# Kernel tuning notes

Hardware: AMD Instinct MI355X
Metric: run time of the kernel (lower is better)

## Reference

```python
import jax, jax.numpy as jnp
import numpy as np
import math

H = 16          # num heads
D = 64          # size_per_head
HID = H * D     # 1024
ROT = 32        # rotary_hsize <= D//2


def setup_inputs() -> dict:
    key = jax.random.key(0)
    ks = jax.random.split(key, 10)
    B, S = 2, 2048
    x = jax.random.normal(ks[0], (B, S, HID), dtype=jnp.float32)
    sinusoids = jax.random.normal(ks[1], (B, 2, S, ROT), dtype=jnp.float32)
    attention_bias = jnp.zeros((B, 1, S, S), dtype=jnp.float32)
    scale = 1.0 / math.sqrt(HID)
    Wq = jax.random.normal(ks[2], (HID, HID), dtype=jnp.float32) * scale
    bq = jnp.zeros((HID,), dtype=jnp.float32)
    Wk = jax.random.normal(ks[3], (HID, HID), dtype=jnp.float32) * scale
    bk = jnp.zeros((HID,), dtype=jnp.float32)
    Wv = jax.random.normal(ks[4], (HID, HID), dtype=jnp.float32) * scale
    bv = jnp.zeros((HID,), dtype=jnp.float32)
    Wo = jax.random.normal(ks[5], (HID, HID), dtype=jnp.float32) * scale
    return {"x": x, "sinusoids": sinusoids, "attention_bias": attention_bias,
            "Wq": Wq, "bq": bq, "Wk": Wk, "bk": bk, "Wv": Wv, "bv": bv, "Wo": Wo}


def _apply_rotary(qk, sin, cos):
    # qk: [B,S,H,D]; sin/cos: [B,S,1,ROT]
    r = qk[..., :ROT]
    # stack([-even, odd], -1).reshape -> interleaved (-x0, x1, -x2, x3, ...)
    rt = jnp.stack([-r[..., ::2], r[..., 1::2]], axis=-1).reshape(r.shape)
    return jnp.concatenate([r * cos + rt * sin, qk[..., ROT:]], axis=-1)


def reference(x, sinusoids, attention_bias, Wq, bq, Wk, bk, Wv, bv, Wo):
    B, S, _ = x.shape
    q = (x @ Wq + bq).reshape(B, S, H, D)
    k = (x @ Wk + bk).reshape(B, S, H, D)
    v = (x @ Wv + bv).reshape(B, S, H, D)
    sin = sinusoids[..., 0, :, None, :]  # [B,S,1,ROT]
    cos = sinusoids[..., 1, :, None, :]
    q = _apply_rotary(q, sin, cos)
    k = _apply_rotary(k, sin, cos)
    q = q / math.sqrt(D)
    scores = jnp.einsum('bqhd,bkhd->bhqk', q, k) + attention_bias
    probs = jax.nn.softmax(scores, axis=-1)
    out = jnp.einsum('bhqk,bkhd->bqhd', probs, v).reshape(B, S, HID)
    return out @ Wo
```

## Files before the change

### kernel.cpp

```cpp
#include <hip/hip_runtime.h>
#include <hip/hip_bf16.h>

#define H_   16
#define D_   64
#define HID  1024
#define S_   2048
#define B_   2
#define M_   (B_*S_)
#define ROT  32
#define LOG2E 1.44269504088896341f
#define QSCALE (0.125f * LOG2E)

typedef __bf16 bf16x8 __attribute__((ext_vector_type(8)));
typedef float  f32x4  __attribute__((ext_vector_type(4)));

#define XB_OFF   0u
#define WQT_OFF  (8u<<20)
#define WKT_OFF  (10u<<20)
#define WVT_OFF  (12u<<20)
#define WOT_OFF  (14u<<20)
#define F_OFF    (16u<<20)
#define QH_OFF   ((16u<<20) + (1u<<19))
#define KH_OFF   (QH_OFF + (8u<<20))
#define VT_OFF   (KH_OFF + (8u<<20))
#define AB_OFF   (VT_OFF + (8u<<20))

__device__ __forceinline__ float fexp2(float x) {
#if __has_builtin(__builtin_amdgcn_exp2f)
  return __builtin_amdgcn_exp2f(x);
#else
  return __expf(x * 0.69314718055994531f);
#endif
}

__device__ __forceinline__ unsigned pk2(float a, float b) {
  union { unsigned u; __bf16 h[2]; } w;
  w.h[0] = (__bf16)a; w.h[1] = (__bf16)b;
  return w.u;
}

__global__ __launch_bounds__(256) void prep_kernel(const float* __restrict__ x,
                                                   const float* __restrict__ sinu,
                                                   const float* __restrict__ abias,
                                                   const float* __restrict__ W0, const float* __restrict__ W1,
                                                   const float* __restrict__ W2, const float* __restrict__ W3,
                                                   __hip_bfloat16* __restrict__ xb,
                                                   float* __restrict__ F,
                                                   __hip_bfloat16* __restrict__ T0, __hip_bfloat16* __restrict__ T1,
                                                   __hip_bfloat16* __restrict__ T2, __hip_bfloat16* __restrict__ T3,
                                                   int* __restrict__ flag) {
  __shared__ float tile[32][33];
  int idx = blockIdx.x;
  int tid = threadIdx.x;
  if (idx < 4096) {
    int i = (idx * 256 + tid) * 4;
    float4 v = *(const float4*)(x + i);
    union { __hip_bfloat16 h[4]; uint2 u; } o;
    o.h[0] = __float2bfloat16(v.x);
    o.h[1] = __float2bfloat16(v.y);
    o.h[2] = __float2bfloat16(v.z);
    o.h[3] = __float2bfloat16(v.w);
    *(uint2*)(xb + i) = o.u;
  } else if (idx < 4608) {
    int i = (idx - 4096) * 256 + tid;
    int d  = i & (ROT-1);
    int bs = i >> 5;
    int s  = bs & (S_-1);
    int b  = bs >> 11;
    float sn = sinu[(((size_t)b*2 + 0)*S_ + s)*ROT + d];
    float cs = sinu[(((size_t)b*2 + 1)*S_ + s)*ROT + d];
    F[i] = cs + ((d & 1) ? sn : -sn);
  } else if (idx < 8704) {
    int widx = idx - 4608;
    int z    = widx >> 10;
    int rem  = widx & 1023;
    const float* W = (z==0) ? W0 : (z==1) ? W1 : (z==2) ? W2 : W3;
    __hip_bfloat16* T = (z==0) ? T0 : (z==1) ? T1 : (z==2) ? T2 : T3;
    int bx = (rem & 31) * 32;
    int by = (rem >> 5) * 32;
    int tx = tid & 31, ty = tid >> 5;
    #pragma unroll
    for (int i = 0; i < 4; i++)
      tile[ty + i*8][tx] = W[(size_t)(by + ty + i*8)*HID + bx + tx];
    __syncthreads();
    #pragma unroll
    for (int i = 0; i < 4; i++)
      T[(size_t)(bx + ty + i*8)*HID + by + tx] = __float2bfloat16(tile[tx][ty + i*8]);
  } else {
    size_t i = ((size_t)(idx - 8704) * 256 + tid) * 16;
    const uint4* p = (const uint4*)(abias + i);
    unsigned acc = 0;
    #pragma unroll
    for (int j = 0; j < 4; j++) {
      uint4 u = p[j];
      acc |= u.x | u.y | u.z | u.w;
    }
    if (acc) *flag = 1;
  }
}

template<int MODE>
__global__ __launch_bounds__(256) void gemm128(const __hip_bfloat16* __restrict__ A,
                                               const __hip_bfloat16* __restrict__ Bt,
                                               const float* __restrict__ bq,
                                               const float* __restrict__ bk,
                                               const float* __restrict__ bv,
                                               const float* __restrict__ F,
                                               __hip_bfloat16* __restrict__ Qh,
                                               __hip_bfloat16* __restrict__ Kh,
                                               __hip_bfloat16* __restrict__ Vt,
                                               float* __restrict__ outf) {
  __shared__ __align__(16) __bf16 Asm[2][128*32];
  __shared__ __align__(16) __bf16 Bsm[2][128*32];
  int tid  = threadIdx.x;
  int lane = tid & 63;
  int wv   = tid >> 6;
  int lr   = lane & 15;
  int qd   = lane >> 4;
  int row0 = blockIdx.y * 128;
  int col0 = blockIdx.x * 128;
  int wrow = (wv >> 1) * 64;
  int wcol = (wv & 1) * 64;

  int cg = ((tid & 3) ^ ((tid >> 2) & 3)) * 8;
  const __bf16* Ag = (const __bf16*)A  + (size_t)(row0 + (tid >> 2)) * HID + cg;
  const __bf16* Bg = (const __bf16*)Bt + (size_t)(col0 + (tid >> 2)) * HID + cg;

  f32x4 acc[4][4] = {};

  auto stage = [&](int buf, int k0) {
    __builtin_amdgcn_global_load_lds(Ag + k0,                  &Asm[buf][wv*512],        16, 0, 0);
    __builtin_amdgcn_global_load_lds(Ag + (size_t)64*HID + k0, &Asm[buf][2048 + wv*512], 16, 0, 0);
    __builtin_amdgcn_global_load_lds(Bg + k0,                  &Bsm[buf][wv*512],        16, 0, 0);
    __builtin_amdgcn_global_load_lds(Bg + (size_t)64*HID + k0, &Bsm[buf][2048 + wv*512], 16, 0, 0);
  };

  stage(0, 0);
  int buf = 0;
  for (int k0 = 0; k0 < HID; k0 += 32, buf ^= 1) {
    __syncthreads();
    if (k0 + 32 < HID) stage(buf ^ 1, k0 + 32);
    const __bf16* As = &Asm[buf][0];
    const __bf16* Bs = &Bsm[buf][0];
    bf16x8 a[4], b[4];
    #pragma unroll
    for (int i = 0; i < 4; i++) {
      int row = wrow + i*16 + lr;
      a[i] = *(const bf16x8*)(As + row*32 + ((qd ^ (row & 3)) * 8));
    }
    #pragma unroll
    for (int t = 0; t < 4; t++) {
      int row = wcol + t*16 + lr;
      b[t] = *(const bf16x8*)(Bs + row*32 + ((qd ^ (row & 3)) * 8));
    }
    #pragma unroll
    for (int i = 0; i < 4; i++)
      #pragma unroll
      for (int t = 0; t < 4; t++)
        acc[i][t] = __builtin_amdgcn_mfma_f32_16x16x32_bf16(a[i], b[t], acc[i][t], 0, 0, 0);
  }

  if (MODE == 1) {
    #pragma unroll
    for (int i = 0; i < 4; i++)
      #pragma unroll
      for (int t = 0; t < 4; t++)
        #pragma unroll
        for (int r = 0; r < 4; r++) {
          int m = row0 + wrow + i*16 + qd*4 + r;
          int n = col0 + wcol + t*16 + lr;
          outf[(size_t)m*HID + n] = acc[i][t][r];
        }
    return;
  }

  int proj = col0 >> 10;
  int nb   = (col0 & 1023) + wcol;
  const float* bias = (proj == 0) ? bq : ((proj == 1) ? bk : bv);
  #pragma unroll
  for (int i = 0; i < 4; i++) {
    #pragma unroll
    for (int t = 0; t < 4; t++) {
      int nl = nb + t*16 + lr;
      int h  = nl >> 6, d = nl & 63;
      if (proj == 2) {
        int m0 = row0 + wrow + i*16 + qd*4;
        int b2 = m0 >> 11, s0 = m0 & (S_-1);
        union { uint2 u; __bf16 hh[4]; } w;
        #pragma unroll
        for (int r = 0; r < 4; r++)
          w.hh[r] = (__bf16)(acc[i][t][r] + bias[nl]);
        *(uint2*)((__bf16*)Vt + ((size_t)(b2*H_ + h)*D_ + d)*S_ + s0) = w.u;
      } else {
        __hip_bfloat16* dst = (proj == 0) ? Qh : Kh;
        #pragma unroll
        for (int r = 0; r < 4; r++) {
          int m = row0 + wrow + i*16 + qd*4 + r;
          int b2 = m >> 11, s = m & (S_-1);
          float v = acc[i][t][r] + bias[nl];
          if (d < ROT) v *= F[(size_t)(b2*S_ + s)*ROT + d];
          if (proj == 0) v *= QSCALE;
          dst[((size_t)(b2*H_ + h)*S_ + s)*D_ + d] = __float2bfloat16(v);
        }
      }
    }
  }
}

#define PSTRIDE 72
__global__ __launch_bounds__(256) void flash_kernel(const __hip_bfloat16* __restrict__ Qh,
                                                    const __hip_bfloat16* __restrict__ Kh,
                                                    const __hip_bfloat16* __restrict__ Vt,
                                                    const float* __restrict__ abias,
                                                    const int* __restrict__ flag,
                                                    __hip_bfloat16* __restrict__ Ab) {
  __shared__ __align__(16) __bf16 Ksm[2][64*64];
  __shared__ __align__(16) __bf16 Vsm[2][64*64];
  __shared__ __align__(16) __bf16 Pb[4][32*PSTRIDE];
  int tid  = threadIdx.x;
  int lane = tid & 63;
  int wv   = tid >> 6;
  int lr   = lane & 15;
  int qd   = lane >> 4;
  int idx  = blockIdx.x;
  int xcd  = idx & 7;
  int slot = idx >> 3;
  int bh   = xcd * 4 + (slot >> 4);
  int qblk = slot & 15;
  int b  = bh >> 4;
  int h  = bh & 15;
  int q0 = qblk * 128 + wv * 32;

  const __bf16* Kbase = (const __bf16*)Kh + (size_t)bh*S_*D_;
  const __bf16* Vbase = (const __bf16*)Vt + (size_t)bh*D_*S_;

  const __bf16* Qp = (const __bf16*)Qh + ((size_t)bh*S_ + q0 + lr)*D_ + qd*8;
  bf16x8 qa00 = *(const bf16x8*)(Qp);
  bf16x8 qa01 = *(const bf16x8*)(Qp + 32);
  bf16x8 qa10 = *(const bf16x8*)(Qp + 16*D_);
  bf16x8 qa11 = *(const bf16x8*)(Qp + 16*D_ + 32);

  int hasbias = *flag;
  const float* bp0 = abias + (size_t)b*S_*S_ + (size_t)(q0 + lr)*S_;
  const float* bp1 = bp0 + (size_t)16*S_;

  int rowb = tid >> 3;
  int cg8  = ((tid & 7) ^ (rowb & 7)) * 8;

  auto stageKV = [&](int bf, int kt2) {
    __builtin_amdgcn_global_load_lds(Kbase + (size_t)(kt2 + rowb)*D_ + cg8,      &Ksm[bf][wv*512],        16, 0, 0);
    __builtin_amdgcn_global_load_lds(Kbase + (size_t)(kt2 + 32 + rowb)*D_ + cg8, &Ksm[bf][2048 + wv*512], 16, 0, 0);
    __builtin_amdgcn_global_load_lds(Vbase + (size_t)rowb*S_ + kt2 + cg8,        &Vsm[bf][wv*512],        16, 0, 0);
    __builtin_amdgcn_global_load_lds(Vbase + (size_t)(32 + rowb)*S_ + kt2 + cg8, &Vsm[bf][2048 + wv*512], 16, 0, 0);
  };

  f32x4 oacc0[4] = {}, oacc1[4] = {};
  float lsum0 = 0.f, lsum1 = 0.f;
  __bf16* P = &Pb[wv][0];
  int sw = lr & 7;

  stageKV(0, 0);
  int buf = 0;
  for (int kt = 0; kt < S_; kt += 64, buf ^= 1) {
    __syncthreads();
    if (kt + 64 < S_) stageKV(buf ^ 1, kt + 64);

    bf16x8 kf0[4], kf1[4];
    #pragma unroll
    for (int c = 0; c < 4; c++) {
      const __bf16* Kr = &Ksm[buf][(c*16 + lr)*64];
      kf0[c] = *(const bf16x8*)(Kr + ((qd       ^ sw) * 8));
      kf1[c] = *(const bf16x8*)(Kr + (((4 + qd) ^ sw) * 8));
    }
    f32x4 s0[4], s1[4];
    #pragma unroll
    for (int c = 0; c < 4; c++) {
      f32x4 z = {};
      z     = __builtin_amdgcn_mfma_f32_16x16x32_bf16(kf0[c], qa00, z, 0, 0, 0);
      s0[c] = __builtin_amdgcn_mfma_f32_16x16x32_bf16(kf1[c], qa01, z, 0, 0, 0);
      f32x4 z2 = {};
      z2    = __builtin_amdgcn_mfma_f32_16x16x32_bf16(kf0[c], qa10, z2, 0, 0, 0);
      s1[c] = __builtin_amdgcn_mfma_f32_16x16x32_bf16(kf1[c], qa11, z2, 0, 0, 0);
    }
    bf16x8 vf0[4], vf1[4];
    #pragma unroll
    for (int t = 0; t < 4; t++) {
      const __bf16* Vr = &Vsm[buf][(t*16 + lr)*64];
      vf0[t] = *(const bf16x8*)(Vr + ((qd       ^ sw) * 8));
      vf1[t] = *(const bf16x8*)(Vr + (((4 + qd) ^ sw) * 8));
    }
    if (hasbias) {
      #pragma unroll
      for (int c = 0; c < 4; c++) {
        float4 b0 = *(const float4*)(bp0 + kt + c*16 + qd*4);
        float4 b1 = *(const float4*)(bp1 + kt + c*16 + qd*4);
        s0[c][0] += b0.x*LOG2E; s0[c][1] += b0.y*LOG2E; s0[c][2] += b0.z*LOG2E; s0[c][3] += b0.w*LOG2E;
        s1[c][0] += b1.x*LOG2E; s1[c][1] += b1.y*LOG2E; s1[c][2] += b1.z*LOG2E; s1[c][3] += b1.w*LOG2E;
      }
    }
    #pragma unroll
    for (int c = 0; c < 4; c++) {
      float p0 = fexp2(s0[c][0]), p1 = fexp2(s0[c][1]), p2 = fexp2(s0[c][2]), p3 = fexp2(s0[c][3]);
      lsum0 += (p0 + p1) + (p2 + p3);
      *(unsigned*)(P + lr*PSTRIDE + c*16 + qd*4)     = pk2(p0, p1);
      *(unsigned*)(P + lr*PSTRIDE + c*16 + qd*4 + 2) = pk2(p2, p3);
      float r0 = fexp2(s1[c][0]), r1 = fexp2(s1[c][1]), r2 = fexp2(s1[c][2]), r3 = fexp2(s1[c][3]);
      lsum1 += (r0 + r1) + (r2 + r3);
      *(unsigned*)(P + (16+lr)*PSTRIDE + c*16 + qd*4)     = pk2(r0, r1);
      *(unsigned*)(P + (16+lr)*PSTRIDE + c*16 + qd*4 + 2) = pk2(r2, r3);
    }
    asm volatile("s_waitcnt lgkmcnt(0)" ::: "memory");
    bf16x8 pb00 = *(const bf16x8*)(P + lr*PSTRIDE + qd*8);
    bf16x8 pb01 = *(const bf16x8*)(P + lr*PSTRIDE + 32 + qd*8);
    bf16x8 pb10 = *(const bf16x8*)(P + (16+lr)*PSTRIDE + qd*8);
    bf16x8 pb11 = *(const bf16x8*)(P + (16+lr)*PSTRIDE + 32 + qd*8);
    #pragma unroll
    for (int t = 0; t < 4; t++) {
      oacc0[t] = __builtin_amdgcn_mfma_f32_16x16x32_bf16(vf0[t], pb00, oacc0[t], 0, 0, 0);
      oacc0[t] = __builtin_amdgcn_mfma_f32_16x16x32_bf16(vf1[t], pb01, oacc0[t], 0, 0, 0);
      oacc1[t] = __builtin_amdgcn_mfma_f32_16x16x32_bf16(vf0[t], pb10, oacc1[t], 0, 0, 0);
      oacc1[t] = __builtin_amdgcn_mfma_f32_16x16x32_bf16(vf1[t], pb11, oacc1[t], 0, 0, 0);
    }
  }

  lsum0 += __shfl_xor(lsum0, 16); lsum0 += __shfl_xor(lsum0, 32);
  lsum1 += __shfl_xor(lsum1, 16); lsum1 += __shfl_xor(lsum1, 32);
  float inv0 = 1.0f / lsum0;
  float inv1 = 1.0f / lsum1;
  size_t ro0 = ((size_t)(b*S_ + q0 + lr))*HID + h*D_;
  size_t ro1 = ((size_t)(b*S_ + q0 + 16 + lr))*HID + h*D_;
  #pragma unroll
  for (int t = 0; t < 4; t++) {
    union { uint2 u; __bf16 hh[4]; } w0, w1;
    #pragma unroll
    for (int r = 0; r < 4; r++) {
      w0.hh[r] = (__bf16)(oacc0[t][r]*inv0);
      w1.hh[r] = (__bf16)(oacc1[t][r]*inv1);
    }
    *(uint2*)((__bf16*)Ab + ro0 + t*16 + qd*4) = w0.u;
    *(uint2*)((__bf16*)Ab + ro1 + t*16 + qd*4) = w1.u;
  }
}

extern "C" void kernel_launch(void* const* d_in, const int* in_sizes, int n_in,
                              void* d_out, int out_size, void* d_ws, size_t ws_size,
                              hipStream_t stream) {
  (void)in_sizes; (void)n_in; (void)out_size; (void)ws_size;
  const float* x     = (const float*)d_in[0];
  const float* sinu  = (const float*)d_in[1];
  const float* abias = (const float*)d_in[2];
  const float* Wq    = (const float*)d_in[3];
  const float* bq    = (const float*)d_in[4];
  const float* Wk    = (const float*)d_in[5];
  const float* bk    = (const float*)d_in[6];
  const float* Wv    = (const float*)d_in[7];
  const float* bv    = (const float*)d_in[8];
  const float* Wo    = (const float*)d_in[9];

  char* ws = (char*)d_ws;
  __hip_bfloat16* Xb  = (__hip_bfloat16*)(ws + XB_OFF);
  __hip_bfloat16* Wqt = (__hip_bfloat16*)(ws + WQT_OFF);
  __hip_bfloat16* Wkt = (__hip_bfloat16*)(ws + WKT_OFF);
  __hip_bfloat16* Wvt = (__hip_bfloat16*)(ws + WVT_OFF);
  __hip_bfloat16* Wot = (__hip_bfloat16*)(ws + WOT_OFF);
  float*          F   = (float*)(ws + F_OFF);
  __hip_bfloat16* Qh  = (__hip_bfloat16*)(ws + QH_OFF);
  __hip_bfloat16* Kh  = (__hip_bfloat16*)(ws + KH_OFF);
  __hip_bfloat16* Vt  = (__hip_bfloat16*)(ws + VT_OFF);
  __hip_bfloat16* Ab  = (__hip_bfloat16*)(ws + AB_OFF);
  int* flag = (int*)d_out;

  hipMemsetAsync(flag, 0, 4, stream);
  prep_kernel<<<10752, 256, 0, stream>>>(x, sinu, abias, Wq, Wk, Wv, Wo,
                                         Xb, F, Wqt, Wkt, Wvt, Wot, flag);

  gemm128<0><<<dim3(3*HID/128, M_/128), 256, 0, stream>>>(
      Xb, Wqt, bq, bk, bv, F, Qh, Kh, Vt, nullptr);

  flash_kernel<<<dim3(512), 256, 0, stream>>>(Qh, Kh, Vt, abias, flag, Ab);

  gemm128<1><<<dim3(HID/128, M_/128), 256, 0, stream>>>(
      Ab, Wot, nullptr, nullptr, nullptr, nullptr, nullptr, nullptr, nullptr, (float*)d_out);
}
```

Before: 229.7 us.

## Software-pipeline PV matmul in flash kernel and use 128x64 tiles for output GEMM

The flash kernel now double-buffers the P tile in LDS and defers each block's P·V MFMAs to the next iteration. They run after the next QK^T scores are computed, so exp/pack work can overlap with matrix ops and the lgkmcnt wait inside the loop goes away. The output projection is split into its own kernel with 128x64 tiles, doubling the block count for better CU occupancy on the 8x32 grid. This costs more LDS for the P buffers and extra V fragment registers carried across iterations.

Measured after the change: 219.8 us. 1.05x faster.

```diff
diff --git a/kernel.cpp b/kernel.cpp
--- a/kernel.cpp
+++ b/kernel.cpp
@@ -99,17 +99,15 @@
   }
 }
 
-template<int MODE>
-__global__ __launch_bounds__(256) void gemm128(const __hip_bfloat16* __restrict__ A,
-                                               const __hip_bfloat16* __restrict__ Bt,
-                                               const float* __restrict__ bq,
-                                               const float* __restrict__ bk,
-                                               const float* __restrict__ bv,
-                                               const float* __restrict__ F,
-                                               __hip_bfloat16* __restrict__ Qh,
-                                               __hip_bfloat16* __restrict__ Kh,
-                                               __hip_bfloat16* __restrict__ Vt,
-                                               float* __restrict__ outf) {
+__global__ __launch_bounds__(256) void qkv_kernel(const __hip_bfloat16* __restrict__ A,
+                                                  const __hip_bfloat16* __restrict__ Bt,
+                                                  const float* __restrict__ bq,
+                                                  const float* __restrict__ bk,
+                                                  const float* __restrict__ bv,
+                                                  const float* __restrict__ F,
+                                                  __hip_bfloat16* __restrict__ Qh,
+                                                  __hip_bfloat16* __restrict__ Kh,
+                                                  __hip_bfloat16* __restrict__ Vt) {
   __shared__ __align__(16) __bf16 Asm[2][128*32];
   __shared__ __align__(16) __bf16 Bsm[2][128*32];
   int tid  = threadIdx.x;
@@ -158,20 +156,6 @@
       #pragma unroll
       for (int t = 0; t < 4; t++)
         acc[i][t] = __builtin_amdgcn_mfma_f32_16x16x32_bf16(a[i], b[t], acc[i][t], 0, 0, 0);
-  }
-
-  if (MODE == 1) {
-    #pragma unroll
-    for (int i = 0; i < 4; i++)
-      #pragma unroll
-      for (int t = 0; t < 4; t++)
-        #pragma unroll
-        for (int r = 0; r < 4; r++) {
-          int m = row0 + wrow + i*16 + qd*4 + r;
-          int n = col0 + wcol + t*16 + lr;
-          outf[(size_t)m*HID + n] = acc[i][t][r];
-        }
-    return;
   }
 
   int proj = col0 >> 10;
@@ -207,6 +191,64 @@
   }
 }
 
+__global__ __launch_bounds__(256) void gemm_o64(const __hip_bfloat16* __restrict__ A,
+                                                const __hip_bfloat16* __restrict__ Bt,
+                                                float* __restrict__ outf) {
+  __shared__ __align__(16) __bf16 Asm[2][128*32];
+  __shared__ __align__(16) __bf16 Bsm[2][64*32];
+  int tid  = threadIdx.x;
+  int lane = tid & 63;
+  int wv   = tid >> 6;
+  int lr   = lane & 15;
+  int qd   = lane >> 4;
+  int row0 = blockIdx.y * 128;
+  int col0 = blockIdx.x * 64;
+  int cg = ((tid & 3) ^ ((tid >> 2) & 3)) * 8;
+  const __bf16* Ag = (const __bf16*)A  + (size_t)(row0 + (tid >> 2)) * HID + cg;
+  const __bf16* Bg = (const __bf16*)Bt + (size_t)(col0 + (tid >> 2)) * HID + cg;
+
+  f32x4 acc[2][4] = {};
+  auto stage = [&](int buf, int k0) {
+    __builtin_amdgcn_global_load_lds(Ag + k0,                  &Asm[buf][wv*512],        16, 0, 0);
+    __builtin_amdgcn_global_load_lds(Ag + (size_t)64*HID + k0, &Asm[buf][2048 + wv*512], 16, 0, 0);
+    __builtin_amdgcn_global_load_lds(Bg + k0,                  &Bsm[buf][wv*512],        16, 0, 0);
+  };
+  stage(0, 0);
+  int buf = 0;
+  for (int k0 = 0; k0 < HID; k0 += 32, buf ^= 1) {
+    __syncthreads();
+    if (k0 + 32 < HID) stage(buf ^ 1, k0 + 32);
+    const __bf16* As = &Asm[buf][0];
+    const __bf16* Bs = &Bsm[buf][0];
+    bf16x8 a[2], b[4];
+    #pragma unroll
+    for (int i = 0; i < 2; i++) {
+      int row = wv*32 + i*16 + lr;
+      a[i] = *(const bf16x8*)(As + row*32 + ((qd ^ (row & 3)) * 8));
+    }
+    #pragma unroll
+    for (int t = 0; t < 4; t++) {
+      int row = t*16 + lr;
+      b[t] = *(const bf16x8*)(Bs + row*32 + ((qd ^ (row & 3)) * 8));
+    }
+    #pragma unroll
+    for (int i = 0; i < 2; i++)
+      #pragma unroll
+      for (int t = 0; t < 4; t++)
+        acc[i][t] = __builtin_amdgcn_mfma_f32_16x16x32_bf16(a[i], b[t], acc[i][t], 0, 0, 0);
+  }
+  #pragma unroll
+  for (int i = 0; i < 2; i++)
+    #pragma unroll
+    for (int t = 0; t < 4; t++)
+      #pragma unroll
+      for (int r = 0; r < 4; r++) {
+        int m = row0 + wv*32 + i*16 + qd*4 + r;
+        int n = col0 + t*16 + lr;
+        outf[(size_t)m*HID + n] = acc[i][t][r];
+      }
+}
+
 #define PSTRIDE 72
 __global__ __launch_bounds__(256) void flash_kernel(const __hip_bfloat16* __restrict__ Qh,
                                                     const __hip_bfloat16* __restrict__ Kh,
@@ -216,7 +258,7 @@
                                                     __hip_bfloat16* __restrict__ Ab) {
   __shared__ __align__(16) __bf16 Ksm[2][64*64];
   __shared__ __align__(16) __bf16 Vsm[2][64*64];
-  __shared__ __align__(16) __bf16 Pb[4][32*PSTRIDE];
+  __shared__ __align__(16) __bf16 Pb[2][4][32*PSTRIDE];
   int tid  = threadIdx.x;
   int lane = tid & 63;
   int wv   = tid >> 6;
@@ -256,7 +298,7 @@
 
   f32x4 oacc0[4] = {}, oacc1[4] = {};
   float lsum0 = 0.f, lsum1 = 0.f;
-  __bf16* P = &Pb[wv][0];
+  bf16x8 vp0[4], vp1[4];
   int sw = lr & 7;
 
   stageKV(0, 0);
@@ -264,6 +306,9 @@
   for (int kt = 0; kt < S_; kt += 64, buf ^= 1) {
     __syncthreads();
     if (kt + 64 < S_) stageKV(buf ^ 1, kt + 64);
+    int pcur = (kt >> 6) & 1;
+    __bf16* Pc = &Pb[pcur][wv][0];
+    const __bf16* Pp = &Pb[pcur ^ 1][wv][0];
 
     bf16x8 kf0[4], kf1[4];
     #pragma unroll
@@ -277,18 +322,34 @@
     for (int c = 0; c < 4; c++) {
       f32x4 z = {};
       z     = __builtin_amdgcn_mfma_f32_16x16x32_bf16(kf0[c], qa00, z, 0, 0, 0);
-      s0[c] = __builtin_amdgcn_mfma_f32_16x16x32_bf16(kf1[c], qa01, z, 0, 0, 0);
+      s0[c] = __builtin_amdgcn_mfma_f32_16x16x32_bf16(kf1[c], qa01, s0[c] = z, 0, 0, 0);
       f32x4 z2 = {};
       z2    = __builtin_amdgcn_mfma_f32_16x16x32_bf16(kf0[c], qa10, z2, 0, 0, 0);
       s1[c] = __builtin_amdgcn_mfma_f32_16x16x32_bf16(kf1[c], qa11, z2, 0, 0, 0);
     }
-    bf16x8 vf0[4], vf1[4];
+
+    bf16x8 vc0[4], vc1[4];
     #pragma unroll
     for (int t = 0; t < 4; t++) {
       const __bf16* Vr = &Vsm[buf][(t*16 + lr)*64];
-      vf0[t] = *(const bf16x8*)(Vr + ((qd       ^ sw) * 8));
-      vf1[t] = *(const bf16x8*)(Vr + (((4 + qd) ^ sw) * 8));
-    }
+      vc0[t] = *(const bf16x8*)(Vr + ((qd       ^ sw) * 8));
+      vc1[t] = *(const bf16x8*)(Vr + (((4 + qd) ^ sw) * 8));
+    }
+
+    if (kt > 0) {
+      bf16x8 pb00 = *(const bf16x8*)(Pp + lr*PSTRIDE + qd*8);
+      bf16x8 pb01 = *(const bf16x8*)(Pp + lr*PSTRIDE + 32 + qd*8);
+      bf16x8 pb10 = *(const bf16x8*)(Pp + (16+lr)*PSTRIDE + qd*8);
+      bf16x8 pb11 = *(const bf16x8*)(Pp + (16+lr)*PSTRIDE + 32 + qd*8);
+      #pragma unroll
+      for (int t = 0; t < 4; t++) {
+        oacc0[t] = __builtin_amdgcn_mfma_f32_16x16x32_bf16(vp0[t], pb00, oacc0[t], 0, 0, 0);
+        oacc0[t] = __builtin_amdgcn_mfma_f32_16x16x32_bf16(vp1[t], pb01, oacc0[t], 0, 0, 0);
+        oacc1[t] = __builtin_amdgcn_mfma_f32_16x16x32_bf16(vp0[t], pb10, oacc1[t], 0, 0, 0);
+        oacc1[t] = __builtin_amdgcn_mfma_f32_16x16x32_bf16(vp1[t], pb11, oacc1[t], 0, 0, 0);
+      }
+    }
+
     if (hasbias) {
       #pragma unroll
       for (int c = 0; c < 4; c++) {
@@ -302,24 +363,31 @@
     for (int c = 0; c < 4; c++) {
       float p0 = fexp2(s0[c][0]), p1 = fexp2(s0[c][1]), p2 = fexp2(s0[c][2]), p3 = fexp2(s0[c][3]);
       lsum0 += (p0 + p1) + (p2 + p3);
-      *(unsigned*)(P + lr*PSTRIDE + c*16 + qd*4)     = pk2(p0, p1);
-      *(unsigned*)(P + lr*PSTRIDE + c*16 + qd*4 + 2) = pk2(p2, p3);
+      *(unsigned*)(Pc + lr*PSTRIDE + c*16 + qd*4)     = pk2(p0, p1);
+      *(unsigned*)(Pc + lr*PSTRIDE + c*16 + qd*4 + 2) = pk2(p2, p3);
       float r0 = fexp2(s1[c][0]), r1 = fexp2(s1[c][1]), r2 = fexp2(s1[c][2]), r3 = fexp2(s1[c][3]);
       lsum1 += (r0 + r1) + (r2 + r3);
-      *(unsigned*)(P + (16+lr)*PSTRIDE + c*16 + qd*4)     = pk2(r0, r1);
-      *(unsigned*)(P + (16+lr)*PSTRIDE + c*16 + qd*4 + 2) = pk2(r2, r3);
-    }
-    asm volatile("s_waitcnt lgkmcnt(0)" ::: "memory");
-    bf16x8 pb00 = *(const bf16x8*)(P + lr*PSTRIDE + qd*8);
-    bf16x8 pb01 = *(const bf16x8*)(P + lr*PSTRIDE + 32 + qd*8);
-    bf16x8 pb10 = *(const bf16x8*)(P + (16+lr)*PSTRIDE + qd*8);
-    bf16x8 pb11 = *(const bf16x8*)(P + (16+lr)*PSTRIDE + 32 + qd*8);
+      *(unsigned*)(Pc + (16+lr)*PSTRIDE + c*16 + qd*4)     = pk2(r0, r1);
+      *(unsigned*)(Pc + (16+lr)*PSTRIDE + c*16 + qd*4 + 2) = pk2(r2, r3);
+    }
+
+    #pragma unroll
+    for (int t = 0; t < 4; t++) { vp0[t] = vc0[t]; vp1[t] = vc1[t]; }
+  }
+
+  asm volatile("s_waitcnt lgkmcnt(0)" ::: "memory");
+  {
+    const __bf16* Pl = &Pb[((S_/64 - 1)) & 1][wv][0];
+    bf16x8 pb00 = *(const bf16x8*)(Pl + lr*PSTRIDE + qd*8);
+    bf16x8 pb01 = *(const bf16x8*)(Pl + lr*PSTRIDE + 32 + qd*8);
+    bf16x8 pb10 = *(const bf16x8*)(Pl + (16+lr)*PSTRIDE + qd*8);
+    bf16x8 pb11 = *(const bf16x8*)(Pl + (16+lr)*PSTRIDE + 32 + qd*8);
     #pragma unroll
     for (int t = 0; t < 4; t++) {
-      oacc0[t] = __builtin_amdgcn_mfma_f32_16x16x32_bf16(vf0[t], pb00, oacc0[t], 0, 0, 0);
-      oacc0[t] = __builtin_amdgcn_mfma_f32_16x16x32_bf16(vf1[t], pb01, oacc0[t], 0, 0, 0);
-      oacc1[t] = __builtin_amdgcn_mfma_f32_16x16x32_bf16(vf0[t], pb10, oacc1[t], 0, 0, 0);
-      oacc1[t] = __builtin_amdgcn_mfma_f32_16x16x32_bf16(vf1[t], pb11, oacc1[t], 0, 0, 0);
+      oacc0[t] = __builtin_amdgcn_mfma_f32_16x16x32_bf16(vp0[t], pb00, oacc0[t], 0, 0, 0);
+      oacc0[t] = __builtin_amdgcn_mfma_f32_16x16x32_bf16(vp1[t], pb01, oacc0[t], 0, 0, 0);
+      oacc1[t] = __builtin_amdgcn_mfma_f32_16x16x32_bf16(vp0[t], pb10, oacc1[t], 0, 0, 0);
+      oacc1[t] = __builtin_amdgcn_mfma_f32_16x16x32_bf16(vp1[t], pb11, oacc1[t], 0, 0, 0);
     }
   }
 
@@ -374,11 +442,10 @@
   prep_kernel<<<10752, 256, 0, stream>>>(x, sinu, abias, Wq, Wk, Wv, Wo,
                                          Xb, F, Wqt, Wkt, Wvt, Wot, flag);
 
-  gemm128<0><<<dim3(3*HID/128, M_/128), 256, 0, stream>>>(
-      Xb, Wqt, bq, bk, bv, F, Qh, Kh, Vt, nullptr);
+  qkv_kernel<<<dim3(3*HID/128, M_/128), 256, 0, stream>>>(
+      Xb, Wqt, bq, bk, bv, F, Qh, Kh, Vt);
 
   flash_kernel<<<dim3(512), 256, 0, stream>>>(Qh, Kh, Vt, abias, flag, Ab);
 
-  gemm128<1><<<dim3(HID/128, M_/128), 256, 0, stream>>>(
-      Ab, Wot, nullptr, nullptr, nullptr, nullptr, nullptr, nullptr, nullptr, (float*)d_out);
-}
+  gemm_o64<<<dim3(HID/64, M_/128), 256, 0, stream>>>(Ab, Wot, (float*)d_out);
+}
```
